# Optimization experiments

Measured on AMD Instinct MI355X. Metric: run time of the kernel, lower is better.

Reference implementation:

```python
import jax, jax.numpy as jnp
import numpy as np
from jax import lax

B, C_IN, C_OUT, H, W = 32, 64, 128, 112, 112
EPS = 1e-5
DW_THRESH = 4.0
PW_THRESH = 0.001


def setup_inputs() -> dict:
    key = jax.random.key(0)
    ks = jax.random.split(key, 13)
    inp = {
        "x": jax.random.normal(ks[0], (B, C_IN, H, W), jnp.float32) * 2.0,
        "dw_w": jax.random.normal(ks[1], (C_IN, 1, 3, 3), jnp.float32) * 0.3,
        "dw_b": jax.random.normal(ks[2], (C_IN,), jnp.float32) * 0.1,
        "bn1_g": jax.random.uniform(ks[3], (C_IN,), jnp.float32, 0.5, 3.5),
        "bn1_b": jax.random.normal(ks[4], (C_IN,), jnp.float32) * 0.1,
        "bn1_m": jax.random.normal(ks[5], (C_IN,), jnp.float32) * 0.1,
        "bn1_v": jax.random.uniform(ks[6], (C_IN,), jnp.float32, 0.5, 1.5),
        "pw_w": jax.random.normal(ks[7], (C_OUT, C_IN), jnp.float32) * 0.1,
        "pw_b": jax.random.normal(ks[8], (C_OUT,), jnp.float32) * 0.1,
        "bn2_g": jax.random.uniform(ks[9], (C_OUT,), jnp.float32, 0.5, 1.5),
        "bn2_b": jax.random.normal(ks[10], (C_OUT,), jnp.float32) * 0.1,
        "bn2_m": jax.random.normal(ks[11], (C_OUT,), jnp.float32) * 0.1,
        "bn2_v": jax.random.uniform(ks[12], (C_OUT,), jnp.float32, 0.5, 1.5),
    }
    return inp


def _bn(x, g, b, m, v):
    # inference-mode BatchNorm2d over channel axis 1
    inv = g * lax.rsqrt(v + EPS)
    return x * inv[None, :, None, None] + (b - m * inv)[None, :, None, None]


def _channel_cut(x, thresh):
    # zero each (batch, channel) plane whose max |value| over HxW is < thresh
    max_abs = jnp.max(jnp.abs(x), axis=(2, 3), keepdims=True)  # [B, C, 1, 1]
    return jnp.where(max_abs < thresh, 0.0, x)


def reference(x, dw_w, dw_b, bn1_g, bn1_b, bn1_m, bn1_v,
              pw_w, pw_b, bn2_g, bn2_b, bn2_m, bn2_v):
    # depthwise 3x3 conv, padding=1, groups=C_IN
    y = lax.conv_general_dilated(
        x, dw_w, window_strides=(1, 1), padding=[(1, 1), (1, 1)],
        dimension_numbers=("NCHW", "OIHW", "NCHW"),
        feature_group_count=C_IN)
    y = y + dw_b[None, :, None, None]
    y = jax.nn.relu(_bn(y, bn1_g, bn1_b, bn1_m, bn1_v))
    y = _channel_cut(y, DW_THRESH)
    # pointwise 1x1 conv == channel contraction
    z = jnp.einsum("bchw,oc->bohw", y, pw_w) + pw_b[None, :, None, None]
    z = jax.nn.relu(_bn(z, bn2_g, bn2_b, bn2_m, bn2_v))
    z = _channel_cut(z, PW_THRESH)
    return z
```

## Files before the change

kernel.cpp:

```cpp
#include <hip/hip_runtime.h>
#include <hip/hip_bf16.h>

#define EPS 1e-5f
#define DW_THRESH 4.0f
#define PW_THRESH 0.001f

typedef __bf16 bf16x4 __attribute__((ext_vector_type(4)));
typedef __bf16 bf16x8 __attribute__((ext_vector_type(8)));
typedef float f32x4 __attribute__((ext_vector_type(4)));

__global__ __launch_bounds__(256, 4) void k_dw(
    const float* __restrict__ x, const float* __restrict__ dww, const float* __restrict__ dwb,
    const float* __restrict__ g1, const float* __restrict__ b1,
    const float* __restrict__ m1, const float* __restrict__ v1,
    const float* __restrict__ zp,
    __bf16* __restrict__ ybuf, unsigned* __restrict__ flags_y)
{
    __shared__ float xs[4][19][128];
    __shared__ float wsc[4][9];
    __shared__ float bi1s[4];

    const int s   = blockIdx.x;
    const int cg  = blockIdx.y;
    const int b   = blockIdx.z;
    const int tid = threadIdx.x;
    const int h0  = s * 16;

    if (tid < 36) {
        int c = tid / 9, k = tid % 9;
        int ch = cg * 4 + c;
        float inv = g1[ch] * rsqrtf(v1[ch] + EPS);
        wsc[c][k] = dww[ch * 9 + k] * inv;
        if (k == 0) bi1s[c] = dwb[ch] * inv + b1[ch] - m1[ch] * inv;
    }
    if (tid < 16) xs[tid >> 2][0][124 + (tid & 3)] = 0.f;

    const int lane  = tid & 63;
    const int wid   = tid >> 6;
    const int lane5 = lane & 31;
    const int half  = lane >> 5;
    const float* xc_base = x + ((long)(b * 64 + cg * 4) * 12544);
#pragma unroll
    for (int issue = 0; issue < 9; ++issue) {
        int rowIdx0 = issue * 8 + wid * 2;
        int c0 = rowIdx0 / 18;
        int j0 = rowIdx0 - c0 * 18;
        int h  = h0 - 1 + j0 + half;
        const float* src = ((unsigned)h < 112u && lane5 < 28)
            ? (xc_base + c0 * 12544 + h * 112 + lane5 * 4)
            : (zp + lane5 * 4);
        __builtin_amdgcn_global_load_lds(
            (const __attribute__((address_space(1))) void*)src,
            (__attribute__((address_space(3))) void*)(&xs[c0][1 + j0][0]),
            16, 0, 0);
    }
    __syncthreads();

    float cmax[4] = {0.f, 0.f, 0.f, 0.f};
    const int hwbase = h0 * 112;

#pragma unroll
    for (int it = 0; it < 2; ++it) {
        int qid = it * 256 + tid;
        if (qid >= 448) break;
        int r  = qid / 28;
        int w0 = (qid - r * 28) * 4;

        float yv[4][4];
#pragma unroll
        for (int c = 0; c < 4; ++c) {
            float a0 = 0.f, a1 = 0.f, a2 = 0.f, a3 = 0.f;
#pragma unroll
            for (int dh = 0; dh < 3; ++dh) {
                const float* row = &xs[c][1 + r + dh][0];
                f32x4 A = *reinterpret_cast<const f32x4*>(row + w0 - 4);
                f32x4 B = *reinterpret_cast<const f32x4*>(row + w0);
                f32x4 C = *reinterpret_cast<const f32x4*>(row + w0 + 4);
                float k0 = wsc[c][dh * 3 + 0];
                float k1 = wsc[c][dh * 3 + 1];
                float k2 = wsc[c][dh * 3 + 2];
                a0 = fmaf(k0, A[3], fmaf(k1, B[0], fmaf(k2, B[1], a0)));
                a1 = fmaf(k0, B[0], fmaf(k1, B[1], fmaf(k2, B[2], a1)));
                a2 = fmaf(k0, B[1], fmaf(k1, B[2], fmaf(k2, B[3], a2)));
                a3 = fmaf(k0, B[2], fmaf(k1, B[3], fmaf(k2, C[0], a3)));
            }
            float bi = bi1s[c];
            yv[c][0] = fmaxf(a0 + bi, 0.f);
            yv[c][1] = fmaxf(a1 + bi, 0.f);
            yv[c][2] = fmaxf(a2 + bi, 0.f);
            yv[c][3] = fmaxf(a3 + bi, 0.f);
            cmax[c] = fmaxf(cmax[c],
                      fmaxf(fmaxf(yv[c][0], yv[c][1]), fmaxf(yv[c][2], yv[c][3])));
        }

        int hw    = hwbase + r * 112 + w0;
        int hwblk = hw >> 4;
        int l16   = hw & 15;
        long base = (((long)(b * 784 + hwblk) * 16 + cg) * 16 + l16) * 4;
        bf16x8 pk0 = { (__bf16)yv[0][0], (__bf16)yv[1][0], (__bf16)yv[2][0], (__bf16)yv[3][0],
                       (__bf16)yv[0][1], (__bf16)yv[1][1], (__bf16)yv[2][1], (__bf16)yv[3][1] };
        bf16x8 pk1 = { (__bf16)yv[0][2], (__bf16)yv[1][2], (__bf16)yv[2][2], (__bf16)yv[3][2],
                       (__bf16)yv[0][3], (__bf16)yv[1][3], (__bf16)yv[2][3], (__bf16)yv[3][3] };
        *reinterpret_cast<bf16x8*>(ybuf + base)     = pk0;
        *reinterpret_cast<bf16x8*>(ybuf + base + 8) = pk1;
    }

#pragma unroll
    for (int c = 0; c < 4; ++c) {
        float m = cmax[c];
#pragma unroll
        for (int d = 1; d < 64; d <<= 1)
            m = fmaxf(m, __shfl_xor(m, d, 64));
        if (lane == 0)
            atomicMax(&flags_y[b * 64 + cg * 4 + c], __float_as_uint(m));
    }
}

__global__ __launch_bounds__(256) void k_pw(
    const float* __restrict__ pww, const float* __restrict__ pwb,
    const float* __restrict__ g2, const float* __restrict__ b2,
    const float* __restrict__ m2, const float* __restrict__ v2,
    const __bf16* __restrict__ ybuf, const unsigned* __restrict__ flags_y,
    float* __restrict__ out, unsigned* __restrict__ flags_z)
{
    __shared__ __bf16 wl[128][72];
    __shared__ float s2[128], bb2[128];
    __shared__ float keepf[64];
    __shared__ unsigned pmz[128];

    const int t   = blockIdx.x;
    const int b   = blockIdx.y;
    const int tid = threadIdx.x;
    const int hw0 = t * 128;

    if (tid < 64)
        keepf[tid] = (__uint_as_float(flags_y[b * 64 + tid]) < DW_THRESH) ? 0.f : 1.f;
    if (tid < 128) {
        float inv = g2[tid] * rsqrtf(v2[tid] + EPS);
        s2[tid]  = inv;
        bb2[tid] = pwb[tid] * inv + b2[tid] - m2[tid] * inv;
        pmz[tid] = 0u;
    }
    __syncthreads();
    for (int i = tid; i < 8192; i += 256) {
        int o = i >> 6, c = i & 63;
        wl[o][c] = (__bf16)(pww[i] * keepf[c]);
    }
    __syncthreads();

    const int wid = tid >> 6, lane = tid & 63;
    const int wm = wid >> 1, wn = wid & 1;
    const int g = lane >> 4, l16 = lane & 15;

    bf16x8 af[4][2];
#pragma unroll
    for (int m = 0; m < 4; ++m)
#pragma unroll
        for (int kb = 0; kb < 2; ++kb)
            af[m][kb] = *reinterpret_cast<const bf16x8*>(&wl[64 * wm + 16 * m + l16][32 * kb + 8 * g]);

    bf16x8 bfr[4][2];
    const int hwblk0 = (hw0 >> 4) + 4 * wn;
#pragma unroll
    for (int q = 0; q < 4; ++q)
#pragma unroll
        for (int kb = 0; kb < 2; ++kb) {
            long rb = ((long)(b * 784 + hwblk0 + q)) * 16;
            int grp = kb * 8 + 2 * g;
            bf16x4 lo = *reinterpret_cast<const bf16x4*>(ybuf + (rb + grp)     * 64 + l16 * 4);
            bf16x4 hi = *reinterpret_cast<const bf16x4*>(ybuf + (rb + grp + 1) * 64 + l16 * 4);
            bfr[q][kb] = (bf16x8){ lo[0], lo[1], lo[2], lo[3],
                                   hi[0], hi[1], hi[2], hi[3] };
        }

    f32x4 acc[4][4];
#pragma unroll
    for (int m = 0; m < 4; ++m)
#pragma unroll
        for (int q = 0; q < 4; ++q)
            acc[m][q] = (f32x4){0.f, 0.f, 0.f, 0.f};

#pragma unroll
    for (int kb = 0; kb < 2; ++kb)
#pragma unroll
        for (int m = 0; m < 4; ++m)
#pragma unroll
            for (int q = 0; q < 4; ++q)
                acc[m][q] = __builtin_amdgcn_mfma_f32_16x16x32_bf16(
                    af[m][kb], bfr[q][kb], acc[m][q], 0, 0, 0);

#pragma unroll
    for (int m = 0; m < 4; ++m) {
#pragma unroll
        for (int r = 0; r < 4; ++r) {
            int o = 64 * wm + 16 * m + 4 * g + r;
            float sc = s2[o], bi = bb2[o];
            float mx = 0.f;
#pragma unroll
            for (int q = 0; q < 4; ++q) {
                float val = fmaxf(fmaf(acc[m][q][r], sc, bi), 0.f);
                mx = fmaxf(mx, val);
                out[(b * 128 + o) * 12544 + hw0 + 64 * wn + 16 * q + l16] = val;
            }
#pragma unroll
            for (int d = 1; d < 16; d <<= 1)
                mx = fmaxf(mx, __shfl_xor(mx, d, 64));
            if (l16 == 0)
                atomicMax(&pmz[o], __float_as_uint(mx));
        }
    }
    __syncthreads();
    if (tid < 128)
        atomicMax(&flags_z[b * 128 + tid], pmz[tid]);
}

__global__ __launch_bounds__(256) void k_cut(
    const unsigned* __restrict__ flags_z, float* __restrict__ out)
{
    int p = blockIdx.x;
    if (__uint_as_float(flags_z[p]) >= PW_THRESH) return;
    int base = p * 12544;
    for (int i = threadIdx.x; i < 12544; i += 256)
        out[base + i] = 0.f;
}

extern "C" void kernel_launch(void* const* d_in, const int* in_sizes, int n_in,
                              void* d_out, int out_size, void* d_ws, size_t ws_size,
                              hipStream_t stream)
{
    const float* x   = (const float*)d_in[0];
    const float* dww = (const float*)d_in[1];
    const float* dwb = (const float*)d_in[2];
    const float* g1  = (const float*)d_in[3];
    const float* b1  = (const float*)d_in[4];
    const float* m1  = (const float*)d_in[5];
    const float* v1  = (const float*)d_in[6];
    const float* pww = (const float*)d_in[7];
    const float* pwb = (const float*)d_in[8];
    const float* g2  = (const float*)d_in[9];
    const float* b2  = (const float*)d_in[10];
    const float* m2  = (const float*)d_in[11];
    const float* v2  = (const float*)d_in[12];
    float* out = (float*)d_out;

    unsigned char* ws = (unsigned char*)d_ws;
    unsigned* flags_y = (unsigned*)ws;
    unsigned* flags_z = (unsigned*)(ws + 8192);
    const float* zp   = (const float*)(ws + 24576);
    __bf16* ybuf      = (__bf16*)(ws + 65536);

    hipMemsetAsync(ws, 0, 25600, stream);

    dim3 gdw(7, 16, 32);
    k_dw<<<gdw, 256, 0, stream>>>(x, dww, dwb, g1, b1, m1, v1, zp, ybuf, flags_y);

    dim3 gpw(98, 32);
    k_pw<<<gpw, 256, 0, stream>>>(pww, pwb, g2, b2, m2, v2, ybuf, flags_y, out, flags_z);

    k_cut<<<4096, 256, 0, stream>>>(flags_z, out);
}
```

Baseline: 117.1 us.

## Compute two output rows per thread in depthwise conv and vectorize pointwise stores

The depthwise kernel now has each of 224 threads compute two adjacent output rows, so the four input rows it reads from shared memory serve both rows instead of being reloaded. The pointwise kernel swaps the MFMA operands so each lane holds four consecutive spatial outputs for one channel. That allows 16-byte vectorized output stores and a shorter shuffle reduction for the channel max. Weight staging is also vectorized to float4 loads. In exchange, more registers are live per thread and fewer threads do compute in the depthwise kernel.

```diff
diff --git a/kernel.cpp b/kernel.cpp
--- a/kernel.cpp
+++ b/kernel.cpp
@@ -59,50 +59,71 @@
     float cmax[4] = {0.f, 0.f, 0.f, 0.f};
     const int hwbase = h0 * 112;
 
-#pragma unroll
-    for (int it = 0; it < 2; ++it) {
-        int qid = it * 256 + tid;
-        if (qid >= 448) break;
-        int r  = qid / 28;
-        int w0 = (qid - r * 28) * 4;
-
-        float yv[4][4];
+    if (tid < 224) {
+        const int rp = tid / 28;
+        const int wq = tid - rp * 28;
+        const int r0 = rp * 2;
+        const int w0 = wq * 4;
+
+        float y0[4][4], y1[4][4];
 #pragma unroll
         for (int c = 0; c < 4; ++c) {
-            float a0 = 0.f, a1 = 0.f, a2 = 0.f, a3 = 0.f;
-#pragma unroll
-            for (int dh = 0; dh < 3; ++dh) {
-                const float* row = &xs[c][1 + r + dh][0];
-                f32x4 A = *reinterpret_cast<const f32x4*>(row + w0 - 4);
-                f32x4 B = *reinterpret_cast<const f32x4*>(row + w0);
-                f32x4 C = *reinterpret_cast<const f32x4*>(row + w0 + 4);
-                float k0 = wsc[c][dh * 3 + 0];
-                float k1 = wsc[c][dh * 3 + 1];
-                float k2 = wsc[c][dh * 3 + 2];
-                a0 = fmaf(k0, A[3], fmaf(k1, B[0], fmaf(k2, B[1], a0)));
-                a1 = fmaf(k0, B[0], fmaf(k1, B[1], fmaf(k2, B[2], a1)));
-                a2 = fmaf(k0, B[1], fmaf(k1, B[2], fmaf(k2, B[3], a2)));
-                a3 = fmaf(k0, B[2], fmaf(k1, B[3], fmaf(k2, C[0], a3)));
+            float a00 = 0.f, a01 = 0.f, a02 = 0.f, a03 = 0.f;
+            float a10 = 0.f, a11 = 0.f, a12 = 0.f, a13 = 0.f;
+#pragma unroll
+            for (int dh2 = 0; dh2 < 4; ++dh2) {
+                const float* row = &xs[c][1 + r0 + dh2][0];
+                f32x4 A  = *reinterpret_cast<const f32x4*>(row + w0 - 4);
+                f32x4 Bv = *reinterpret_cast<const f32x4*>(row + w0);
+                f32x4 Cv = *reinterpret_cast<const f32x4*>(row + w0 + 4);
+                if (dh2 < 3) {
+                    float k0 = wsc[c][dh2 * 3 + 0];
+                    float k1 = wsc[c][dh2 * 3 + 1];
+                    float k2 = wsc[c][dh2 * 3 + 2];
+                    a00 = fmaf(k0, A[3],  fmaf(k1, Bv[0], fmaf(k2, Bv[1], a00)));
+                    a01 = fmaf(k0, Bv[0], fmaf(k1, Bv[1], fmaf(k2, Bv[2], a01)));
+                    a02 = fmaf(k0, Bv[1], fmaf(k1, Bv[2], fmaf(k2, Bv[3], a02)));
+                    a03 = fmaf(k0, Bv[2], fmaf(k1, Bv[3], fmaf(k2, Cv[0], a03)));
+                }
+                if (dh2 > 0) {
+                    float k0 = wsc[c][(dh2 - 1) * 3 + 0];
+                    float k1 = wsc[c][(dh2 - 1) * 3 + 1];
+                    float k2 = wsc[c][(dh2 - 1) * 3 + 2];
+                    a10 = fmaf(k0, A[3],  fmaf(k1, Bv[0], fmaf(k2, Bv[1], a10)));
+                    a11 = fmaf(k0, Bv[0], fmaf(k1, Bv[1], fmaf(k2, Bv[2], a11)));
+                    a12 = fmaf(k0, Bv[1], fmaf(k1, Bv[2], fmaf(k2, Bv[3], a12)));
+                    a13 = fmaf(k0, Bv[2], fmaf(k1, Bv[3], fmaf(k2, Cv[0], a13)));
+                }
             }
             float bi = bi1s[c];
-            yv[c][0] = fmaxf(a0 + bi, 0.f);
-            yv[c][1] = fmaxf(a1 + bi, 0.f);
-            yv[c][2] = fmaxf(a2 + bi, 0.f);
-            yv[c][3] = fmaxf(a3 + bi, 0.f);
-            cmax[c] = fmaxf(cmax[c],
-                      fmaxf(fmaxf(yv[c][0], yv[c][1]), fmaxf(yv[c][2], yv[c][3])));
-        }
-
-        int hw    = hwbase + r * 112 + w0;
-        int hwblk = hw >> 4;
-        int l16   = hw & 15;
-        long base = (((long)(b * 784 + hwblk) * 16 + cg) * 16 + l16) * 4;
-        bf16x8 pk0 = { (__bf16)yv[0][0], (__bf16)yv[1][0], (__bf16)yv[2][0], (__bf16)yv[3][0],
-                       (__bf16)yv[0][1], (__bf16)yv[1][1], (__bf16)yv[2][1], (__bf16)yv[3][1] };
-        bf16x8 pk1 = { (__bf16)yv[0][2], (__bf16)yv[1][2], (__bf16)yv[2][2], (__bf16)yv[3][2],
-                       (__bf16)yv[0][3], (__bf16)yv[1][3], (__bf16)yv[2][3], (__bf16)yv[3][3] };
-        *reinterpret_cast<bf16x8*>(ybuf + base)     = pk0;
-        *reinterpret_cast<bf16x8*>(ybuf + base + 8) = pk1;
+            y0[c][0] = fmaxf(a00 + bi, 0.f);
+            y0[c][1] = fmaxf(a01 + bi, 0.f);
+            y0[c][2] = fmaxf(a02 + bi, 0.f);
+            y0[c][3] = fmaxf(a03 + bi, 0.f);
+            y1[c][0] = fmaxf(a10 + bi, 0.f);
+            y1[c][1] = fmaxf(a11 + bi, 0.f);
+            y1[c][2] = fmaxf(a12 + bi, 0.f);
+            y1[c][3] = fmaxf(a13 + bi, 0.f);
+#pragma unroll
+            for (int i = 0; i < 4; ++i)
+                cmax[c] = fmaxf(cmax[c], fmaxf(y0[c][i], y1[c][i]));
+        }
+
+        int hwq  = hwbase + r0 * 112 + w0;
+        long baseA = (((long)(b * 784 + (hwq >> 4)) * 16 + cg) * 16 + (hwq & 15)) * 4;
+        long baseB = baseA + 7L * 1024;
+        bf16x8 p0 = { (__bf16)y0[0][0], (__bf16)y0[1][0], (__bf16)y0[2][0], (__bf16)y0[3][0],
+                      (__bf16)y0[0][1], (__bf16)y0[1][1], (__bf16)y0[2][1], (__bf16)y0[3][1] };
+        bf16x8 p1 = { (__bf16)y0[0][2], (__bf16)y0[1][2], (__bf16)y0[2][2], (__bf16)y0[3][2],
+                      (__bf16)y0[0][3], (__bf16)y0[1][3], (__bf16)y0[2][3], (__bf16)y0[3][3] };
+        bf16x8 p2 = { (__bf16)y1[0][0], (__bf16)y1[1][0], (__bf16)y1[2][0], (__bf16)y1[3][0],
+                      (__bf16)y1[0][1], (__bf16)y1[1][1], (__bf16)y1[2][1], (__bf16)y1[3][1] };
+        bf16x8 p3 = { (__bf16)y1[0][2], (__bf16)y1[1][2], (__bf16)y1[2][2], (__bf16)y1[3][2],
+                      (__bf16)y1[0][3], (__bf16)y1[1][3], (__bf16)y1[2][3], (__bf16)y1[3][3] };
+        *reinterpret_cast<bf16x8*>(ybuf + baseA)     = p0;
+        *reinterpret_cast<bf16x8*>(ybuf + baseA + 8) = p1;
+        *reinterpret_cast<bf16x8*>(ybuf + baseB)     = p2;
+        *reinterpret_cast<bf16x8*>(ybuf + baseB + 8) = p3;
     }
 
 #pragma unroll
@@ -142,9 +163,20 @@
         pmz[tid] = 0u;
     }
     __syncthreads();
-    for (int i = tid; i < 8192; i += 256) {
-        int o = i >> 6, c = i & 63;
-        wl[o][c] = (__bf16)(pww[i] * keepf[c]);
+    {
+        const f32x4* pw4 = reinterpret_cast<const f32x4*>(pww);
+#pragma unroll
+        for (int k = 0; k < 8; ++k) {
+            int i = k * 256 + tid;
+            f32x4 wv = pw4[i];
+            int o  = i >> 4;
+            int c4 = (i & 15) << 2;
+            bf16x4 bv = { (__bf16)(wv[0] * keepf[c4 + 0]),
+                          (__bf16)(wv[1] * keepf[c4 + 1]),
+                          (__bf16)(wv[2] * keepf[c4 + 2]),
+                          (__bf16)(wv[3] * keepf[c4 + 3]) };
+            *reinterpret_cast<bf16x4*>(&wl[o][c4]) = bv;
+        }
     }
     __syncthreads();
 
@@ -187,27 +219,28 @@
 #pragma unroll
             for (int q = 0; q < 4; ++q)
                 acc[m][q] = __builtin_amdgcn_mfma_f32_16x16x32_bf16(
-                    af[m][kb], bfr[q][kb], acc[m][q], 0, 0, 0);
+                    bfr[q][kb], af[m][kb], acc[m][q], 0, 0, 0);
 
 #pragma unroll
     for (int m = 0; m < 4; ++m) {
-#pragma unroll
-        for (int r = 0; r < 4; ++r) {
-            int o = 64 * wm + 16 * m + 4 * g + r;
-            float sc = s2[o], bi = bb2[o];
-            float mx = 0.f;
-#pragma unroll
-            for (int q = 0; q < 4; ++q) {
-                float val = fmaxf(fmaf(acc[m][q][r], sc, bi), 0.f);
-                mx = fmaxf(mx, val);
-                out[(b * 128 + o) * 12544 + hw0 + 64 * wn + 16 * q + l16] = val;
+        int o = 64 * wm + 16 * m + l16;
+        float sc = s2[o], bi = bb2[o];
+        float mx = 0.f;
+        long pbase = (long)(b * 128 + o) * 12544 + hw0 + 64 * wn + 4 * g;
+#pragma unroll
+        for (int q = 0; q < 4; ++q) {
+            f32x4 v;
+#pragma unroll
+            for (int r = 0; r < 4; ++r) {
+                v[r] = fmaxf(fmaf(acc[m][q][r], sc, bi), 0.f);
+                mx = fmaxf(mx, v[r]);
             }
-#pragma unroll
-            for (int d = 1; d < 16; d <<= 1)
-                mx = fmaxf(mx, __shfl_xor(mx, d, 64));
-            if (l16 == 0)
-                atomicMax(&pmz[o], __float_as_uint(mx));
-        }
+            *reinterpret_cast<f32x4*>(out + pbase + 16 * q) = v;
+        }
+        mx = fmaxf(mx, __shfl_xor(mx, 16, 64));
+        mx = fmaxf(mx, __shfl_xor(mx, 32, 64));
+        if (lane < 16)
+            atomicMax(&pmz[o], __float_as_uint(mx));
     }
     __syncthreads();
     if (tid < 128)
```

Measured after the change: 112.1 us. -4.2%, faster.
